# Kernel optimization log

Measured on AMD Instinct MI355X. Metric: run time of the kernel, lower is better.

## Reference

```python
import jax, jax.numpy as jnp
import numpy as np

IGNORE_IDX = -100
DELTA_V = 0.5
DELTA_D = 1.5
PARAM_VAR = 1.0
PARAM_DIST = 1.0
PARAM_REG = 0.001
LOSS_WEIGHT = 1.0
K = 64  # static upper bound on number of instances (matches fill_max of instance_labels)


def setup_inputs() -> dict:
    key = jax.random.key(0)
    k1, k2, k3 = jax.random.split(key, 3)
    B, D, N = 8, 32, 131072
    embedding_logits = jax.random.normal(k1, (B, D, N), dtype=jnp.float32)
    semantic_labels = jax.random.randint(k2, (B, N), 0, 21, dtype=jnp.int64)
    instance_labels = jax.random.randint(k3, (B, N), 0, K, dtype=jnp.int64)
    return {
        "embedding_logits": embedding_logits,
        "semantic_labels": semantic_labels,
        "instance_labels": instance_labels,
        "feature_dim": D,
    }


def _single(x, cls, inst):
    # x: [N, D] embeddings, cls/inst: [N] int labels
    dtype = x.dtype
    valid = cls != IGNORE_IDX
    # points of class 1 are merged into instance 0 (intent of the torch code)
    inst = jnp.where(cls == 1, 0, inst)
    ids = jnp.where(valid, inst, K)  # invalid points -> extra bin K

    counts = jax.ops.segment_sum(valid.astype(dtype), ids, num_segments=K + 1)[:K]
    seg_sum = jax.ops.segment_sum(
        jnp.where(valid[:, None], x, jnp.zeros((), dtype)), ids, num_segments=K + 1
    )[:K]                                            # [K, D]
    mu = seg_sum / (counts[:, None] + 1e-8)          # [K, D] cluster means
    present = counts > 0                             # [K]
    n_inst = jnp.maximum(jnp.sum(present.astype(dtype)), 1.0)

    # intra-cluster variance term (L1 distance to own cluster mean, hinged)
    mu_pt = mu[jnp.clip(ids, 0, K - 1)]              # [N, D]
    d = jnp.sum(jnp.abs(x - mu_pt), axis=1)          # [N]
    d = jnp.square(jnp.maximum(d - DELTA_V, 0.0)) * valid.astype(dtype)
    l_var_seg = jax.ops.segment_sum(d, ids, num_segments=K + 1)[:K] / (counts + 1e-8)
    l_var = jnp.sum(l_var_seg) / n_inst

    # inter-cluster distance term over distinct present cluster pairs
    pdist = jnp.sum(jnp.abs(mu[:, None, :] - mu[None, :, :]), axis=-1)  # [K, K]
    pair_mask = present[:, None] & present[None, :] & ~jnp.eye(K, dtype=bool)
    hinge = jnp.square(jnp.maximum(2.0 * DELTA_D - pdist, 0.0)) * pair_mask.astype(dtype)
    npairs = jnp.sum(pair_mask.astype(dtype))
    l_dist = jnp.where(npairs > 0, jnp.sum(hinge) / jnp.maximum(npairs, 1.0), 0.0)

    # regularization: mean L1 norm of present cluster means
    l_reg = jnp.sum(jnp.sum(jnp.abs(mu), axis=1) * present.astype(dtype)) / n_inst

    l_var = PARAM_VAR * l_var
    l_dist = PARAM_DIST * l_dist
    l_reg = PARAM_REG * l_reg
    loss = LOSS_WEIGHT * (l_var + l_dist + l_reg)
    return loss, l_var, l_dist, l_reg


def reference(embedding_logits, semantic_labels, instance_labels, feature_dim):
    # embedding_logits: [B, D, N] -> per-point embeddings [B, N, D]
    x = jnp.transpose(embedding_logits, (0, 2, 1))
    loss, l_var, l_dist, l_reg = jax.vmap(_single)(x, semantic_labels, instance_labels)
    return (
        jnp.mean(loss),
        jnp.mean(l_var),
        jnp.mean(l_dist),
        jnp.mean(l_reg),
    )
```

## Files before the change

### kernel.cpp

```cpp
#include <hip/hip_runtime.h>


typedef unsigned char uchar;
typedef __attribute__((ext_vector_type(8)))  short bf16x8;
typedef __attribute__((ext_vector_type(16))) float f32x16;

#define IGNORE_IDX (-100)

constexpr int B = 8;
constexpr int D = 32;
constexpr int K = 64;
constexpr int NPTS = 131072;
constexpr int BPB  = 128;
constexpr int SPAN = 1024;
constexpr float DELTA_V = 0.5f;
constexpr float TWO_DELTA_D = 3.0f;
constexpr float PARAM_REG = 0.001f;

constexpr size_t OFF_CNT = (size_t)B * 2048;
constexpr size_t OFF_VS  = OFF_CNT + (size_t)B * K;
constexpr size_t OFF_ID  = OFF_VS  + (size_t)B * K;
constexpr size_t ZERO_FLOATS = OFF_ID;

__device__ inline unsigned bfpack(unsigned a0, unsigned a1) {
    return __builtin_amdgcn_perm(a1, a0, 0x07060302u);
}

__global__ __launch_bounds__(256) void k1_fused(
    const float* __restrict__ x, const int* __restrict__ sem,
    const int* __restrict__ inst, uchar* __restrict__ id8,
    int* __restrict__ cnt, float* __restrict__ musum)
{
    __shared__ float s_part[4][2048];
    __shared__ unsigned s_id4[256];
    __shared__ int s_cnt[K];
    const int t = threadIdx.x, w = t >> 6, L = t & 63;
    const int g = L >> 5, ln = L & 31;
    const unsigned lnu = (unsigned)ln, lnp32 = (unsigned)(ln + 32);
    const int blk = blockIdx.x, b = blk >> 7, sp = blk & (BPB - 1);

    if (t < K) s_cnt[t] = 0;
    __syncthreads();

    {
        const size_t off = (size_t)b * NPTS + sp * SPAN + t * 4;
        const int4 c4 = *(const int4*)(sem + off);
        const int4 i4 = *(const int4*)(inst + off);
        const int cl[4] = {c4.x, c4.y, c4.z, c4.w};
        const int il[4] = {i4.x, i4.y, i4.z, i4.w};
        unsigned wrd = 0;
#pragma unroll
        for (int j = 0; j < 4; ++j) {
            const bool v = (cl[j] != IGNORE_IDX);
            int q = (cl[j] == 1) ? 0 : il[j];
            q = (q < 0) ? 0 : (q > K - 1 ? K - 1 : q);
            if (v) atomicAdd(&s_cnt[q], 1);
            wrd |= (v ? (unsigned)q : 255u) << (8 * j);
        }
        s_id4[t] = wrd;
        *(unsigned*)(id8 + off) = wrd;
    }

    f32x16 acc0, acc1;
#pragma unroll
    for (int i = 0; i < 16; ++i) { acc0[i] = 0.f; acc1[i] = 0.f; }
    __syncthreads();

    const unsigned* xrow = (const unsigned*)(x + (size_t)b * D * NPTS
                                             + (size_t)ln * NPTS + sp * SPAN);
    for (int it = 0; it < SPAN / 64; ++it) {
        const int n0 = (it * 4 + w) * 16 + g * 8;
        const uint2 idq = *(const uint2*)(&s_id4[n0 >> 2]);
        const uint4 xa = *(const uint4*)(xrow + n0);
        const uint4 xc = *(const uint4*)(xrow + n0 + 4);

        union { unsigned u[4]; bf16x8 v; } Ah, B0, B1;
        Ah.u[0] = bfpack(xa.x + 0x8000u, xa.y + 0x8000u);
        Ah.u[1] = bfpack(xa.z + 0x8000u, xa.w + 0x8000u);
        Ah.u[2] = bfpack(xc.x + 0x8000u, xc.y + 0x8000u);
        Ah.u[3] = bfpack(xc.z + 0x8000u, xc.w + 0x8000u);
#pragma unroll
        for (int p = 0; p < 4; ++p) {
            const unsigned pair = ((p < 2) ? idq.x : idq.y) >> ((p & 1) * 16);
            const unsigned e0 = pair & 255u, e1 = (pair >> 8) & 255u;
            unsigned r0 = (e0 == lnu)   ? 0x3F80u : 0u;
            unsigned r1 = (e0 == lnp32) ? 0x3F80u : 0u;
            if (e1 == lnu)   r0 |= 0x3F800000u;
            if (e1 == lnp32) r1 |= 0x3F800000u;
            B0.u[p] = r0; B1.u[p] = r1;
        }
        acc0 = __builtin_amdgcn_mfma_f32_32x32x16_bf16(Ah.v, B0.v, acc0, 0, 0, 0);
        acc1 = __builtin_amdgcn_mfma_f32_32x32x16_bf16(Ah.v, B1.v, acc1, 0, 0, 0);
    }

#pragma unroll
    for (int r = 0; r < 16; ++r) {
        const int row = (r & 3) + 8 * (r >> 2) + 4 * g;
        s_part[w][row * 64 + ln]      = acc0[r];
        s_part[w][row * 64 + ln + 32] = acc1[r];
    }
    __syncthreads();

    float* dst = musum + (size_t)b * 2048;
    for (int i = t; i < 2048; i += 256)
        unsafeAtomicAdd(&dst[i],
            s_part[0][i] + s_part[1][i] + s_part[2][i] + s_part[3][i]);
    if (t < K) {
        const int c = s_cnt[t];
        if (c) atomicAdd(&cnt[b * K + t], c);
    }
}

__global__ __launch_bounds__(256) void k3_var(
    const float* __restrict__ x, const uchar* __restrict__ id8,
    const float* __restrict__ musum, const int* __restrict__ cnt,
    float* __restrict__ vsum)
{
    __shared__ float s_mu[2048];
    __shared__ float s_var[K];
    const int t = threadIdx.x;
    const int blk = blockIdx.x, b = blk >> 7, sp = blk & (BPB - 1);

    if (t < K) s_var[t] = 0.f;
    for (int i = t; i < 2048; i += 256)
        s_mu[i] = musum[(size_t)b * 2048 + i]
                / ((float)cnt[b * K + (i & 63)] + 1e-8f);

    const unsigned idw = *(const unsigned*)(id8 + (size_t)b * NPTS + sp * SPAN + t * 4);
    int q[4]; bool val[4];
#pragma unroll
    for (int j = 0; j < 4; ++j) {
        const unsigned e = (idw >> (8 * j)) & 255u;
        val[j] = (e < 64u);
        q[j] = (int)(e & 63u);
    }
    __syncthreads();

    const float* xp = x + (size_t)b * D * NPTS + sp * SPAN + t * 4;
    float s0 = 0.f, s1 = 0.f, s2 = 0.f, s3 = 0.f;
#pragma unroll
    for (int d = 0; d < D; ++d) {
        const float4 xv = *(const float4*)(xp + (size_t)d * NPTS);
        s0 += fabsf(xv.x - s_mu[d * 64 + q[0]]);
        s1 += fabsf(xv.y - s_mu[d * 64 + q[1]]);
        s2 += fabsf(xv.z - s_mu[d * 64 + q[2]]);
        s3 += fabsf(xv.w - s_mu[d * 64 + q[3]]);
    }

    const float ss[4] = {s0, s1, s2, s3};
#pragma unroll
    for (int j = 0; j < 4; ++j) {
        if (val[j]) {
            const float h = fmaxf(ss[j] - DELTA_V, 0.f);
            if (h > 0.f) unsafeAtomicAdd(&s_var[q[j]], h * h);
        }
    }
    __syncthreads();
    if (t < K) {
        const float v = s_var[t];
        if (v != 0.f) unsafeAtomicAdd(&vsum[b * K + t], v);
    }
}

__device__ float block_reduce_sum512(float v, float* s_buf) {
    for (int o = 32; o > 0; o >>= 1) v += __shfl_down(v, o, 64);
    const int wid  = threadIdx.x >> 6;
    const int lane = threadIdx.x & 63;
    if (lane == 0) s_buf[wid] = v;
    __syncthreads();
    float r = 0.f;
    if (threadIdx.x == 0)
        for (int w = 0; w < 8; ++w) r += s_buf[w];
    __syncthreads();
    return r;
}

__global__ __launch_bounds__(512) void k4_final(const float* __restrict__ musum,
                                                const int* __restrict__ cnt,
                                                const float* __restrict__ vsum,
                                                float* __restrict__ out)
{
    const int b = blockIdx.x;
    __shared__ float s_mu[K][D + 1];
    __shared__ float s_cnt[K];
    __shared__ float s_red[8];

    const int t = threadIdx.x;
    if (t < K) s_cnt[t] = (float)cnt[b * K + t];
    for (int i = t; i < K * D; i += 512) {
        const int d = i >> 6, k = i & 63;
        s_mu[k][d] = musum[(size_t)b * 2048 + i]
                   / ((float)cnt[b * K + k] + 1e-8f);
    }
    __syncthreads();

    float distPart = 0.f;
    for (int p = t; p < K * K; p += 512) {
        const int i = p >> 6, j = p & 63;
        if (i != j && s_cnt[i] > 0.f && s_cnt[j] > 0.f) {
            float dsum = 0.f;
#pragma unroll
            for (int d = 0; d < D; ++d) dsum += fabsf(s_mu[i][d] - s_mu[j][d]);
            const float h = fmaxf(TWO_DELTA_D - dsum, 0.f);
            distPart += h * h;
        }
    }
    float regPart = 0.f;
    for (int i = t; i < K * D; i += 512) {
        const int k = i & 63;
        if (s_cnt[k] > 0.f) regPart += fabsf(s_mu[k][i >> 6]);
    }
    float varPart = 0.f, npPart = 0.f;
    if (t < K) {
        varPart = vsum[b * K + t] / (s_cnt[t] + 1e-8f);
        npPart  = (s_cnt[t] > 0.f) ? 1.f : 0.f;
    }

    const float distSum = block_reduce_sum512(distPart, s_red);
    const float regSum  = block_reduce_sum512(regPart,  s_red);
    const float varSum  = block_reduce_sum512(varPart,  s_red);
    const float npSum   = block_reduce_sum512(npPart,   s_red);

    if (t == 0) {
        const float n_inst = fmaxf(npSum, 1.0f);
        const float npairs = npSum * npSum - npSum;
        const float l_var  = varSum / n_inst;
        const float l_dist = (npairs > 0.f) ? (distSum / fmaxf(npairs, 1.0f)) : 0.f;
        const float l_reg  = PARAM_REG * (regSum / n_inst);
        const float invB   = 1.0f / (float)B;
        unsafeAtomicAdd(out + 0, (l_var + l_dist + l_reg) * invB);
        unsafeAtomicAdd(out + 1, l_var  * invB);
        unsafeAtomicAdd(out + 2, l_dist * invB);
        unsafeAtomicAdd(out + 3, l_reg  * invB);
    }
}

extern "C" void kernel_launch(void* const* d_in, const int* in_sizes, int n_in,
                              void* d_out, int out_size, void* d_ws, size_t ws_size,
                              hipStream_t stream) {
    const float* x    = (const float*)d_in[0];
    const int*   sem  = (const int*)d_in[1];
    const int*   inst = (const int*)d_in[2];
    float*       out  = (float*)d_out;
    float*       ws   = (float*)d_ws;

    float* musum = ws;
    int*   cnt   = (int*)(ws + OFF_CNT);
    float* vsum  = ws + OFF_VS;
    uchar* id8   = (uchar*)(ws + OFF_ID);

    hipMemsetAsync(ws, 0, ZERO_FLOATS * sizeof(float), stream);
    hipMemsetAsync(out, 0, (size_t)out_size * sizeof(float), stream);

    k1_fused<<<dim3(B * BPB), dim3(256), 0, stream>>>(x, sem, inst, id8, cnt, musum);
    k3_var  <<<dim3(B * BPB), dim3(256), 0, stream>>>(x, id8, musum, cnt, vsum);
    k4_final<<<dim3(B), dim3(512), 0, stream>>>(musum, cnt, vsum, out);
}
```

Before: 254.7 us.

## Replace global atomics with per-block partials and a dedicated reduce kernel

k1 now writes each block's 2048-cell partial sums and counts to private workspace slots instead of doing global float and int atomics. A new k2_reduce kernel sums the 128 partials per batch, computes the means once, and zeroes vsum and the output, which removes both memsets. k3 and k4 then read precomputed means instead of dividing again. The cost is an extra kernel launch and about 8 MB of partial-sum traffic written and reread, traded against atomic contention and two memset launches.

```diff
diff --git a/kernel.cpp b/kernel.cpp
--- a/kernel.cpp
+++ b/kernel.cpp
@@ -17,10 +17,11 @@
 constexpr float TWO_DELTA_D = 3.0f;
 constexpr float PARAM_REG = 0.001f;
 
-constexpr size_t OFF_CNT = (size_t)B * 2048;
+constexpr size_t OFF_CP  = (size_t)B * BPB * 2048;
+constexpr size_t OFF_MU  = OFF_CP + (size_t)B * BPB * K;
+constexpr size_t OFF_CNT = OFF_MU + (size_t)B * 2048;
 constexpr size_t OFF_VS  = OFF_CNT + (size_t)B * K;
-constexpr size_t OFF_ID  = OFF_VS  + (size_t)B * K;
-constexpr size_t ZERO_FLOATS = OFF_ID;
+constexpr size_t OFF_ID  = OFF_VS + (size_t)B * K;
 
 __device__ inline unsigned bfpack(unsigned a0, unsigned a1) {
     return __builtin_amdgcn_perm(a1, a0, 0x07060302u);
@@ -29,7 +30,7 @@
 __global__ __launch_bounds__(256) void k1_fused(
     const float* __restrict__ x, const int* __restrict__ sem,
     const int* __restrict__ inst, uchar* __restrict__ id8,
-    int* __restrict__ cnt, float* __restrict__ musum)
+    int* __restrict__ cnt_part, float* __restrict__ part)
 {
     __shared__ float s_part[4][2048];
     __shared__ unsigned s_id4[256];
@@ -101,20 +102,59 @@
     }
     __syncthreads();
 
-    float* dst = musum + (size_t)b * 2048;
+    float* dst = part + (size_t)blk * 2048;
     for (int i = t; i < 2048; i += 256)
-        unsafeAtomicAdd(&dst[i],
-            s_part[0][i] + s_part[1][i] + s_part[2][i] + s_part[3][i]);
+        dst[i] = s_part[0][i] + s_part[1][i] + s_part[2][i] + s_part[3][i];
+    if (t < K) cnt_part[blk * K + t] = s_cnt[t];
+}
+
+__global__ __launch_bounds__(256) void k2_reduce(
+    const float* __restrict__ part, const int* __restrict__ cnt_part,
+    float* __restrict__ mu, int* __restrict__ cnt,
+    float* __restrict__ vsum, float* __restrict__ out)
+{
+    __shared__ float4 s_acc[256];
+    __shared__ float s_cntB[K];
+    const int t = threadIdx.x, bb = blockIdx.x;
+    const int b = bb >> 3;
+    const int cell0 = (bb & 7) * 256 + (t & 63) * 4;
+    const int jq = t >> 6;
+
+    float4 acc = make_float4(0.f, 0.f, 0.f, 0.f);
+    const float* pb = part + (size_t)b * BPB * 2048 + cell0;
+    for (int j = jq * 32; j < jq * 32 + 32; ++j) {
+        const float4 v = *(const float4*)(pb + (size_t)j * 2048);
+        acc.x += v.x; acc.y += v.y; acc.z += v.z; acc.w += v.w;
+    }
+    s_acc[t] = acc;
+
     if (t < K) {
-        const int c = s_cnt[t];
-        if (c) atomicAdd(&cnt[b * K + t], c);
+        int ci = 0;
+        for (int j = 0; j < BPB; ++j)
+            ci += cnt_part[(size_t)(b * BPB + j) * K + t];
+        s_cntB[t] = (float)ci;
+        if ((bb & 7) == 0) cnt[b * K + t] = ci;
+    }
+    if (t >= 64 && t < 72) vsum[bb * 8 + (t - 64)] = 0.f;
+    if (bb == 0 && t >= 128 && t < 132) out[t - 128] = 0.f;
+    __syncthreads();
+
+    if (t < 64) {
+        const float4 a0 = s_acc[t], a1 = s_acc[t + 64],
+                     a2 = s_acc[t + 128], a3 = s_acc[t + 192];
+        const int c0 = (bb & 7) * 256 + t * 4;
+        float4 m;
+        m.x = (a0.x + a1.x + a2.x + a3.x) / (s_cntB[(c0 + 0) & 63] + 1e-8f);
+        m.y = (a0.y + a1.y + a2.y + a3.y) / (s_cntB[(c0 + 1) & 63] + 1e-8f);
+        m.z = (a0.z + a1.z + a2.z + a3.z) / (s_cntB[(c0 + 2) & 63] + 1e-8f);
+        m.w = (a0.w + a1.w + a2.w + a3.w) / (s_cntB[(c0 + 3) & 63] + 1e-8f);
+        *(float4*)(mu + (size_t)b * 2048 + c0) = m;
     }
 }
 
 __global__ __launch_bounds__(256) void k3_var(
     const float* __restrict__ x, const uchar* __restrict__ id8,
-    const float* __restrict__ musum, const int* __restrict__ cnt,
-    float* __restrict__ vsum)
+    const float* __restrict__ mu, float* __restrict__ vsum)
 {
     __shared__ float s_mu[2048];
     __shared__ float s_var[K];
@@ -123,8 +163,7 @@
 
     if (t < K) s_var[t] = 0.f;
     for (int i = t; i < 2048; i += 256)
-        s_mu[i] = musum[(size_t)b * 2048 + i]
-                / ((float)cnt[b * K + (i & 63)] + 1e-8f);
+        s_mu[i] = mu[(size_t)b * 2048 + i];
 
     const unsigned idw = *(const unsigned*)(id8 + (size_t)b * NPTS + sp * SPAN + t * 4);
     int q[4]; bool val[4];
@@ -175,7 +214,7 @@
     return r;
 }
 
-__global__ __launch_bounds__(512) void k4_final(const float* __restrict__ musum,
+__global__ __launch_bounds__(512) void k4_final(const float* __restrict__ mu,
                                                 const int* __restrict__ cnt,
                                                 const float* __restrict__ vsum,
                                                 float* __restrict__ out)
@@ -189,8 +228,7 @@
     if (t < K) s_cnt[t] = (float)cnt[b * K + t];
     for (int i = t; i < K * D; i += 512) {
         const int d = i >> 6, k = i & 63;
-        s_mu[k][d] = musum[(size_t)b * 2048 + i]
-                   / ((float)cnt[b * K + k] + 1e-8f);
+        s_mu[k][d] = mu[(size_t)b * 2048 + i];
     }
     __syncthreads();
 
@@ -244,15 +282,15 @@
     float*       out  = (float*)d_out;
     float*       ws   = (float*)d_ws;
 
-    float* musum = ws;
-    int*   cnt   = (int*)(ws + OFF_CNT);
-    float* vsum  = ws + OFF_VS;
-    uchar* id8   = (uchar*)(ws + OFF_ID);
-
-    hipMemsetAsync(ws, 0, ZERO_FLOATS * sizeof(float), stream);
-    hipMemsetAsync(out, 0, (size_t)out_size * sizeof(float), stream);
-
-    k1_fused<<<dim3(B * BPB), dim3(256), 0, stream>>>(x, sem, inst, id8, cnt, musum);
-    k3_var  <<<dim3(B * BPB), dim3(256), 0, stream>>>(x, id8, musum, cnt, vsum);
-    k4_final<<<dim3(B), dim3(512), 0, stream>>>(musum, cnt, vsum, out);
-}
+    float* part     = ws;
+    int*   cnt_part = (int*)(ws + OFF_CP);
+    float* mu       = ws + OFF_MU;
+    int*   cnt      = (int*)(ws + OFF_CNT);
+    float* vsum     = ws + OFF_VS;
+    uchar* id8      = (uchar*)(ws + OFF_ID);
+
+    k1_fused <<<dim3(B * BPB), dim3(256), 0, stream>>>(x, sem, inst, id8, cnt_part, part);
+    k2_reduce<<<dim3(K),       dim3(256), 0, stream>>>(part, cnt_part, mu, cnt, vsum, out);
+    k3_var   <<<dim3(B * BPB), dim3(256), 0, stream>>>(x, id8, mu, vsum);
+    k4_final <<<dim3(B),       dim3(512), 0, stream>>>(mu, cnt, vsum, out);
+}
```

Measured after the change: 262.8 us. 3.2% more time.

## Stage x tiles through swizzled LDS with register prefetch for coalesced loads

Applied to the files above, without the earlier changes.

The segment-sum kernel stops having each lane read its own feature row directly from global memory. A wave now loads contiguous 256-point chunks per feature row into registers, prefetching the next chunk, converts them to bf16, and writes them into XOR-swizzled LDS. MFMA A-fragments are then read from LDS. This aims for wider, coalesced global reads and to overlap load latency with compute, at the cost of LDS traffic and two barriers per stage. Separately, the reg-term loop index mapping in the final kernel is changed, apparently to fix s_mu indexing.

```diff
diff --git a/kernel.cpp b/kernel.cpp
--- a/kernel.cpp
+++ b/kernel.cpp
@@ -31,7 +31,7 @@
     const int* __restrict__ inst, uchar* __restrict__ id8,
     int* __restrict__ cnt, float* __restrict__ musum)
 {
-    __shared__ float s_part[4][2048];
+    __shared__ __align__(16) char s_mem[32768];
     __shared__ unsigned s_id4[256];
     __shared__ int s_cnt[K];
     const int t = threadIdx.x, w = t >> 6, L = t & 63;
@@ -64,35 +64,57 @@
     f32x16 acc0, acc1;
 #pragma unroll
     for (int i = 0; i < 16; ++i) { acc0[i] = 0.f; acc1[i] = 0.f; }
-    __syncthreads();
-
-    const unsigned* xrow = (const unsigned*)(x + (size_t)b * D * NPTS
-                                             + (size_t)ln * NPTS + sp * SPAN);
-    for (int it = 0; it < SPAN / 64; ++it) {
-        const int n0 = (it * 4 + w) * 16 + g * 8;
-        const uint2 idq = *(const uint2*)(&s_id4[n0 >> 2]);
-        const uint4 xa = *(const uint4*)(xrow + n0);
-        const uint4 xc = *(const uint4*)(xrow + n0 + 4);
-
-        union { unsigned u[4]; bf16x8 v; } Ah, B0, B1;
-        Ah.u[0] = bfpack(xa.x + 0x8000u, xa.y + 0x8000u);
-        Ah.u[1] = bfpack(xa.z + 0x8000u, xa.w + 0x8000u);
-        Ah.u[2] = bfpack(xc.x + 0x8000u, xc.y + 0x8000u);
-        Ah.u[3] = bfpack(xc.z + 0x8000u, xc.w + 0x8000u);
-#pragma unroll
-        for (int p = 0; p < 4; ++p) {
-            const unsigned pair = ((p < 2) ? idq.x : idq.y) >> ((p & 1) * 16);
-            const unsigned e0 = pair & 255u, e1 = (pair >> 8) & 255u;
-            unsigned r0 = (e0 == lnu)   ? 0x3F80u : 0u;
-            unsigned r1 = (e0 == lnp32) ? 0x3F80u : 0u;
-            if (e1 == lnu)   r0 |= 0x3F800000u;
-            if (e1 == lnp32) r1 |= 0x3F800000u;
-            B0.u[p] = r0; B1.u[p] = r1;
-        }
-        acc0 = __builtin_amdgcn_mfma_f32_32x32x16_bf16(Ah.v, B0.v, acc0, 0, 0, 0);
-        acc1 = __builtin_amdgcn_mfma_f32_32x32x16_bf16(Ah.v, B1.v, acc1, 0, 0, 0);
-    }
-
+
+    const unsigned* xb = (const unsigned*)(x + (size_t)b * D * NPTS + sp * SPAN);
+
+    uint4 pf[8];
+#pragma unroll
+    for (int P = 0; P < 8; ++P)
+        pf[P] = *(const uint4*)(xb + (size_t)(P * 4 + w) * NPTS + L * 4);
+
+    for (int st = 0; st < 4; ++st) {
+#pragma unroll
+        for (int P = 0; P < 8; ++P) {
+            const int row = P * 4 + w;
+            const unsigned u0 = bfpack(pf[P].x + 0x8000u, pf[P].y + 0x8000u);
+            const unsigned u1 = bfpack(pf[P].z + 0x8000u, pf[P].w + 0x8000u);
+            const int waddr = row * 512 + (((L >> 1) ^ (row & 7)) * 16) + (L & 1) * 8;
+            *(uint2*)(s_mem + waddr) = make_uint2(u0, u1);
+        }
+        if (st < 3) {
+#pragma unroll
+            for (int P = 0; P < 8; ++P)
+                pf[P] = *(const uint4*)(xb + (size_t)(P * 4 + w) * NPTS
+                                        + (st + 1) * 256 + L * 4);
+        }
+        __syncthreads();
+
+#pragma unroll
+        for (int cc = 0; cc < 4; ++cc) {
+            const int K16 = (w * 4 + cc) * 2 + g;
+            const int raddr = ln * 512 + ((K16 ^ (ln & 7)) * 16);
+            const bf16x8 Af = *(const bf16x8*)(s_mem + raddr);
+
+            const int n0 = st * 256 + (w * 4 + cc) * 16 + g * 8;
+            const uint2 idq = *(const uint2*)(&s_id4[n0 >> 2]);
+            union { unsigned u[4]; bf16x8 v; } B0, B1;
+#pragma unroll
+            for (int p = 0; p < 4; ++p) {
+                const unsigned pair = ((p < 2) ? idq.x : idq.y) >> ((p & 1) * 16);
+                const unsigned e0 = pair & 255u, e1 = (pair >> 8) & 255u;
+                unsigned r0 = (e0 == lnu)   ? 0x3F80u : 0u;
+                unsigned r1 = (e0 == lnp32) ? 0x3F80u : 0u;
+                if (e1 == lnu)   r0 |= 0x3F800000u;
+                if (e1 == lnp32) r1 |= 0x3F800000u;
+                B0.u[p] = r0; B1.u[p] = r1;
+            }
+            acc0 = __builtin_amdgcn_mfma_f32_32x32x16_bf16(Af, B0.v, acc0, 0, 0, 0);
+            acc1 = __builtin_amdgcn_mfma_f32_32x32x16_bf16(Af, B1.v, acc1, 0, 0, 0);
+        }
+        __syncthreads();
+    }
+
+    float (*s_part)[2048] = (float(*)[2048])s_mem;
 #pragma unroll
     for (int r = 0; r < 16; ++r) {
         const int row = (r & 3) + 8 * (r >> 2) + 4 * g;
@@ -207,8 +229,8 @@
     }
     float regPart = 0.f;
     for (int i = t; i < K * D; i += 512) {
-        const int k = i & 63;
-        if (s_cnt[k] > 0.f) regPart += fabsf(s_mu[k][i >> 6]);
+        const int k = i >> 5;
+        if (s_cnt[k] > 0.f) regPart += fabsf(s_mu[k][i & 31]);
     }
     float varPart = 0.f, npPart = 0.f;
     if (t < K) {
```

Measured after the change: 248.1 us. 2.6% less time.
